# Kernel optimization log

Hardware: AMD Instinct MI355X
Metric: run time of the kernel (lower is better)

The kernel has to match this reference:

```python
import jax, jax.numpy as jnp
import numpy as np

B, D, H, K = 8192, 1280, 16384, 64


def setup_inputs() -> dict:
    key = jax.random.key(0)
    k1, k2, k3 = jax.random.split(key, 3)
    x = jax.random.normal(k1, (B, D), dtype=jnp.float32)
    # encoder weight [hidden_dim, input_dim] (torch Linear layout)
    W_enc = jax.random.normal(k2, (H, D), dtype=jnp.float32) * (1.0 / np.sqrt(D))
    b_enc = jnp.zeros((H,), dtype=jnp.float32)
    # decoder weight [input_dim, hidden_dim], unit-norm columns scaled by 0.1
    W_dec = jax.random.normal(k3, (D, H), dtype=jnp.float32)
    W_dec = 0.1 * W_dec / jnp.linalg.norm(W_dec, axis=0, keepdims=True)
    b_dec = jnp.zeros((D,), dtype=jnp.float32)
    b_pre = jnp.zeros((D,), dtype=jnp.float32)
    return {"x": x, "W_enc": W_enc, "b_enc": b_enc, "W_dec": W_dec,
            "b_dec": b_dec, "b_pre": b_pre, "k": K}


def reference(x, W_enc, b_enc, W_dec, b_dec, b_pre, k):
    # --- encode ---
    x_centered = x - b_pre                                   # [B, D]
    pre = jnp.einsum('bd,hd->bh', x_centered, W_enc) + b_enc  # [B, H]
    vals, idx = jax.lax.top_k(pre, k)                        # [B, k]
    rows = jnp.arange(pre.shape[0])[:, None]                 # [B, 1]
    hidden = jnp.zeros_like(pre).at[rows, idx].set(jax.nn.relu(vals))  # [B, H]
    # --- decode ---
    reconstructed = jnp.einsum('bh,dh->bd', hidden, W_dec) + b_dec + b_pre
    # --- losses ---
    reconstruction_loss = jnp.mean((reconstructed - x) ** 2)
    l0 = jnp.mean(jnp.sum((hidden > 0).astype(jnp.float32), axis=-1))
    sparsity_loss = jnp.array(0.0, dtype=jnp.float32)
    loss = reconstruction_loss
    return reconstructed, hidden, loss, reconstruction_loss, sparsity_loss, l0
```

## Files before the change

### kernel.cpp

```cpp
#include <hip/hip_runtime.h>
#include <hip/hip_bf16.h>

constexpr int K_MAX    = 128;
constexpr int S_MAX    = 128;
constexpr int A_MAX    = 256;
constexpr int CAND_MAX = 512;
constexpr int BM = 128, BN = 128, BKF = 16;
constexpr int NBITER = 42;
constexpr int D_MAX   = 2048;
constexpr int H_FIX   = 16384;

typedef __attribute__((ext_vector_type(8))) short bf16x8;
typedef __attribute__((ext_vector_type(8))) unsigned short u16x8;
typedef __attribute__((ext_vector_type(4))) float f32x4;

__device__ inline unsigned short f2bf(float f) {
  unsigned u = __float_as_uint(f);
  return (unsigned short)((u + 0x7fff + ((u >> 16) & 1)) >> 16);
}
__device__ inline unsigned short key_of(float f) {
  unsigned short b = f2bf(f);
  return b ^ ((b & 0x8000) ? 0xFFFF : 0x8000);
}
__device__ inline float val_of_key(unsigned short kk) {
  unsigned short b = (kk & 0x8000) ? (unsigned short)(kk ^ 0x8000)
                                   : (unsigned short)(kk ^ 0xFFFF);
  return __uint_as_float(((unsigned)b) << 16);
}
__device__ inline float bf2f(unsigned short b) {
  return __uint_as_float(((unsigned)b) << 16);
}

__device__ inline int lds_slot(int r, int c) {
  return ((r >> 1) << 4) | ((r & 1) << 3) | (c ^ ((r >> 1) & 7));
}

__global__ __launch_bounds__(256) void prep_xb(
    const float* __restrict__ x, const float* __restrict__ b_pre,
    unsigned short* __restrict__ Xb, int D, size_t total4)
{
  for (size_t i = blockIdx.x * 256 + threadIdx.x; i < total4; i += (size_t)gridDim.x * 256) {
    const size_t e = i * 4;
    const int d = (int)(e % D);
    float4 xv = *reinterpret_cast<const float4*>(x + e);
    float4 bp = *reinterpret_cast<const float4*>(b_pre + d);
    ushort4 o;
    o.x = f2bf(xv.x - bp.x); o.y = f2bf(xv.y - bp.y);
    o.z = f2bf(xv.z - bp.z); o.w = f2bf(xv.w - bp.w);
    *reinterpret_cast<ushort4*>(Xb + e) = o;
  }
}

__global__ __launch_bounds__(256) void prep_wb(
    const float* __restrict__ W, unsigned short* __restrict__ Wb, size_t total4)
{
  for (size_t i = blockIdx.x * 256 + threadIdx.x; i < total4; i += (size_t)gridDim.x * 256) {
    const size_t e = i * 4;
    float4 wv = *reinterpret_cast<const float4*>(W + e);
    ushort4 o;
    o.x = f2bf(wv.x); o.y = f2bf(wv.y); o.z = f2bf(wv.z); o.w = f2bf(wv.w);
    *reinterpret_cast<ushort4*>(Wb + e) = o;
  }
}

__global__ __launch_bounds__(512, 2) void enc_gemm_bf16(
    const unsigned short* __restrict__ Xb, const unsigned short* __restrict__ Wb,
    const float* __restrict__ b_enc, float* __restrict__ pre, int D, int H)
{
  __shared__ unsigned short As[2][2048 * 8];
  __shared__ unsigned short Bs[2][2048 * 8];
  const int tid  = threadIdx.x;
  const int wave = tid >> 6, lane = tid & 63;
  const int m0 = blockIdx.y * 256, n0 = blockIdx.x * 256;
  const int wm = (wave >> 1) * 64;
  const int wn = (wave & 1) * 128;
  const int l16 = lane & 15, lhi = lane >> 4;

  f32x4 acc[4][8];
#pragma unroll
  for (int i = 0; i < 4; ++i)
#pragma unroll
    for (int j = 0; j < 8; ++j) acc[i][j] = (f32x4){0.f, 0.f, 0.f, 0.f};

  const int NT = D / 64;

  auto stageA = [&](int buf, int h, int kb) {
#pragma unroll
    for (int i = 0; i < 2; ++i) {
      const int idx = i * 512 + wave * 64 + lane;
      const int sr = idx >> 4, u = idx & 15;
      const int r  = (sr << 1) | (u >> 3);
      const int ch = (u & 7) ^ (sr & 7);
      __builtin_amdgcn_global_load_lds(
          (const __attribute__((address_space(1))) unsigned int*)
              (Xb + (size_t)(m0 + h * 128 + r) * D + kb + ch * 8),
          (__attribute__((address_space(3))) unsigned int*)
              (&As[buf][(size_t)(h * 1024 + idx) * 8]), 16, 0, 0);
    }
  };
  auto stageBq = [&](int buf, int q, int kb) {
    const int s  = (q & 1) * 512 + wave * 64 + lane;
    const int sr = s >> 4, u = s & 15;
    const int r  = (sr << 1) | (u >> 3);
    const int ch = (u & 7) ^ (sr & 7);
    __builtin_amdgcn_global_load_lds(
        (const __attribute__((address_space(1))) unsigned int*)
            (Wb + (size_t)(n0 + (q >> 1) * 128 + r) * D + kb + ch * 8),
        (__attribute__((address_space(3))) unsigned int*)
            (&Bs[buf][(size_t)((q >> 1) * 1024 + s) * 8]), 16, 0, 0);
  };
  auto readA = [&](int buf, int mi, int kk) -> bf16x8 {
    const int gr = wm + mi * 16 + l16;
    return *reinterpret_cast<const bf16x8*>(
        &As[buf][(size_t)((gr >> 7) * 1024 + lds_slot(gr & 127, kk * 4 + lhi)) * 8]);
  };
  auto readB = [&](int buf, int ni, int kk) -> bf16x8 {
    const int gr = wn + ni * 16 + l16;
    return *reinterpret_cast<const bf16x8*>(
        &Bs[buf][(size_t)((gr >> 7) * 1024 + lds_slot(gr & 127, kk * 4 + lhi)) * 8]);
  };

  stageA(0, 0, 0); stageA(0, 1, 0);
  stageBq(0, 0, 0); stageBq(0, 2, 0);
  stageBq(0, 1, 0); stageBq(0, 3, 0);

  int cur = 0;
  for (int t = 0; t < NT; ++t) {
    const int nxt = cur ^ 1;
    const int kb1 = (t + 1) * 64;
    const bool more = (t + 1 < NT);

    bf16x8 af[4][2], bf[2][2];

    asm volatile("s_waitcnt vmcnt(2)" ::: "memory");
    __builtin_amdgcn_s_barrier();
#pragma unroll
    for (int mi = 0; mi < 4; ++mi)
#pragma unroll
      for (int kk = 0; kk < 2; ++kk) af[mi][kk] = readA(cur, mi, kk);
#pragma unroll
    for (int j = 0; j < 2; ++j)
#pragma unroll
      for (int kk = 0; kk < 2; ++kk) bf[j][kk] = readB(cur, j, kk);
    if (more) stageA(nxt, 0, kb1);
    __builtin_amdgcn_s_setprio(1);
#pragma unroll
    for (int mi = 0; mi < 4; ++mi)
#pragma unroll
      for (int j = 0; j < 2; ++j)
#pragma unroll
        for (int kk = 0; kk < 2; ++kk)
          acc[mi][j] = __builtin_amdgcn_mfma_f32_16x16x32_bf16(af[mi][kk], bf[j][kk], acc[mi][j], 0, 0, 0);
    __builtin_amdgcn_s_setprio(0);

#pragma unroll
    for (int j = 0; j < 2; ++j)
#pragma unroll
      for (int kk = 0; kk < 2; ++kk) bf[j][kk] = readB(cur, 2 + j, kk);
    if (more) stageA(nxt, 1, kb1);
    __builtin_amdgcn_s_setprio(1);
#pragma unroll
    for (int mi = 0; mi < 4; ++mi)
#pragma unroll
      for (int j = 0; j < 2; ++j)
#pragma unroll
        for (int kk = 0; kk < 2; ++kk)
          acc[mi][2 + j] = __builtin_amdgcn_mfma_f32_16x16x32_bf16(af[mi][kk], bf[j][kk], acc[mi][2 + j], 0, 0, 0);
    __builtin_amdgcn_s_setprio(0);

    if (more) { asm volatile("s_waitcnt vmcnt(4)" ::: "memory"); }
    else      { asm volatile("s_waitcnt vmcnt(0)" ::: "memory"); }
    __builtin_amdgcn_s_barrier();
#pragma unroll
    for (int j = 0; j < 2; ++j)
#pragma unroll
      for (int kk = 0; kk < 2; ++kk) bf[j][kk] = readB(cur, 4 + j, kk);
    if (more) { stageBq(nxt, 0, kb1); stageBq(nxt, 2, kb1); }
    __builtin_amdgcn_s_setprio(1);
#pragma unroll
    for (int mi = 0; mi < 4; ++mi)
#pragma unroll
      for (int j = 0; j < 2; ++j)
#pragma unroll
        for (int kk = 0; kk < 2; ++kk)
          acc[mi][4 + j] = __builtin_amdgcn_mfma_f32_16x16x32_bf16(af[mi][kk], bf[j][kk], acc[mi][4 + j], 0, 0, 0);
    __builtin_amdgcn_s_setprio(0);

#pragma unroll
    for (int j = 0; j < 2; ++j)
#pragma unroll
      for (int kk = 0; kk < 2; ++kk) bf[j][kk] = readB(cur, 6 + j, kk);
    if (more) { stageBq(nxt, 1, kb1); stageBq(nxt, 3, kb1); }
    __builtin_amdgcn_s_setprio(1);
#pragma unroll
    for (int mi = 0; mi < 4; ++mi)
#pragma unroll
      for (int j = 0; j < 2; ++j)
#pragma unroll
        for (int kk = 0; kk < 2; ++kk)
          acc[mi][6 + j] = __builtin_amdgcn_mfma_f32_16x16x32_bf16(af[mi][kk], bf[j][kk], acc[mi][6 + j], 0, 0, 0);
    __builtin_amdgcn_s_setprio(0);

    cur = nxt;
  }

#pragma unroll
  for (int ni = 0; ni < 8; ++ni) {
    const int n = n0 + wn + ni * 16 + l16;
    const float be = b_enc[n];
#pragma unroll
    for (int mi = 0; mi < 4; ++mi) {
      const int mbase = m0 + wm + mi * 16 + lhi * 4;
#pragma unroll
      for (int r = 0; r < 4; ++r) {
        unsigned short* prow = (unsigned short*)(pre + (size_t)(mbase + r) * H);
        prow[n] = key_of(acc[mi][ni][r] + be);
      }
    }
  }
}

__global__ __launch_bounds__(256) void topk_classify_keys(
    float* __restrict__ hidden,
    int* __restrict__ sure_ix, float* __restrict__ sure_val, int* __restrict__ sure_cnt,
    int* __restrict__ amb_ix, int* __restrict__ amb_cnt,
    const int* __restrict__ kptr, float delta)
{
  constexpr int H = H_FIX, NC = H_FIX / (256 * 8);
  __shared__ int hist[4096];
  __shared__ int chunk[256];
  __shared__ int misc[8];

  const int tid = threadIdx.x, b = blockIdx.x;
  const int k = min(*kptr, K_MAX);
  float* hrow = hidden + (size_t)b * H;
  const unsigned short* krow = (const unsigned short*)hrow;

  if (tid < 8) misc[tid] = 0;
  for (int i = tid; i < 4096; i += 256) hist[i] = 0;

  u16x8 kv[NC];
#pragma unroll
  for (int i = 0; i < NC; ++i)
    kv[i] = *reinterpret_cast<const u16x8*>(krow + ((size_t)i * 256 + tid) * 8);
  __syncthreads();

  const float4 z4 = {0.f, 0.f, 0.f, 0.f};
  for (int i = tid; i < (H >> 2); i += 256)
    reinterpret_cast<float4*>(hrow)[i] = z4;

#pragma unroll
  for (int i = 0; i < NC; ++i)
#pragma unroll
    for (int j = 0; j < 8; ++j)
      atomicAdd(&hist[((unsigned)(unsigned short)kv[i][j]) >> 4], 1);
  __syncthreads();

  int csum = 0;
#pragma unroll
  for (int j = 0; j < 16; ++j) csum += hist[tid * 16 + j];
  chunk[tid] = csum;
  __syncthreads();
  int gt = 0;
  for (int j = tid + 1; j < 256; ++j) gt += chunk[j];
  {
    int run = gt;
#pragma unroll
    for (int j = 15; j >= 0; --j) {
      const int hc = hist[tid * 16 + j];
      if (run < k && k <= run + hc) { misc[0] = tid * 16 + j; misc[1] = run; }
      run += hc;
    }
  }
  __syncthreads();
  const int b1 = misc[0];
  if (tid < 16) chunk[tid] = 0;
  __syncthreads();
#pragma unroll
  for (int i = 0; i < NC; ++i)
#pragma unroll
    for (int j = 0; j < 8; ++j) {
      const unsigned kk = (unsigned)(unsigned short)kv[i][j];
      if ((int)(kk >> 4) == b1) atomicAdd(&chunk[kk & 15], 1);
    }
  __syncthreads();
  if (tid == 0) {
    int run = misc[1];
    int K16 = b1 << 4;
    for (int j = 15; j >= 0; --j) {
      const int c = chunk[j];
      if (run < k && k <= run + c) K16 = (b1 << 4) | j;
      run += c;
    }
    const float v_lo = val_of_key((unsigned short)K16);
    const float v_hi = val_of_key((unsigned short)min(K16 + 1, 65535));
    const float ulp = v_hi - v_lo;
    const float vs = v_hi + delta;
    const float va = v_lo - ulp - delta;
    int ks = key_of(vs); if (val_of_key((unsigned short)ks) > vs) --ks;
    int ka = key_of(va); if (val_of_key((unsigned short)ka) < va) ++ka;
    misc[2] = ks; misc[3] = ka;
  }
  __syncthreads();
  const unsigned ks = (unsigned)misc[2], ka = (unsigned)misc[3];

#pragma unroll
  for (int i = 0; i < NC; ++i)
#pragma unroll
    for (int j = 0; j < 8; ++j) {
      const unsigned kk = (unsigned)(unsigned short)kv[i][j];
      if (kk > ks) {
        const int p = atomicAdd(&misc[4], 1);
        if (p < S_MAX) {
          const int h = (i * 256 + tid) * 8 + j;
          sure_ix[(size_t)b * S_MAX + p] = h;
          sure_val[(size_t)b * S_MAX + p] = val_of_key((unsigned short)kk);
        }
      } else if (kk >= ka) {
        const int p = atomicAdd(&misc[5], 1);
        if (p < A_MAX) amb_ix[(size_t)b * A_MAX + p] = (i * 256 + tid) * 8 + j;
      }
    }
  __syncthreads();
  if (tid == 0) {
    sure_cnt[b] = min(misc[4], S_MAX);
    amb_cnt[b]  = min(misc[5], A_MAX);
  }
}

__global__ __launch_bounds__(256) void refine_scatter(
    const float* __restrict__ X, const float* __restrict__ b_pre,
    const float* __restrict__ W, const float* __restrict__ b_enc,
    const int* __restrict__ sure_ix, const float* __restrict__ sure_val,
    const int* __restrict__ sure_cnt,
    const int* __restrict__ amb_ix, const int* __restrict__ amb_cnt,
    const int* __restrict__ kptr,
    float* __restrict__ hidden, int* __restrict__ tk_idx, float* __restrict__ tk_val, int D)
{
  constexpr int H = H_FIX;
  __shared__ float  xr[D_MAX];
  __shared__ double asv[A_MAX];
  __shared__ int    aix[A_MAX];
  const int tid = threadIdx.x, b = blockIdx.x;
  const int k = min(*kptr, K_MAX);
  const int S = min(min(sure_cnt[b], S_MAX), k);
  const int A = min(amb_cnt[b], A_MAX);
  float* hrow = hidden + (size_t)b * H;

  for (int d = tid; d < D; d += 256) xr[d] = X[(size_t)b * D + d] - b_pre[d];
  for (int c = tid; c < A; c += 256) aix[c] = amb_ix[(size_t)b * A_MAX + c];

  for (int i = tid; i < S; i += 256) {
    const int h = sure_ix[(size_t)b * S_MAX + i];
    const float v = sure_val[(size_t)b * S_MAX + i];
    const float rv = (v > 0.f) ? v : 0.f;
    hrow[h] = rv;
    tk_idx[(size_t)b * K_MAX + i] = h;
    tk_val[(size_t)b * K_MAX + i] = rv;
  }
  __syncthreads();

  const int wid = tid >> 6, lane = tid & 63;
  for (int c = wid; c < A; c += 4) {
    const int h = aix[c];
    const float* wr = W + (size_t)h * D;
    double s0 = 0.0, s1 = 0.0;
    int i = lane;
    for (; i + 64 < D; i += 128) {
      s0 += (double)xr[i] * (double)wr[i];
      s1 += (double)xr[i + 64] * (double)wr[i + 64];
    }
    if (i < D) s0 += (double)xr[i] * (double)wr[i];
    double s = s0 + s1;
    for (int off = 32; off; off >>= 1) s += __shfl_xor(s, off);
    if (lane == 0) asv[c] = s + (double)b_enc[h];
  }
  __syncthreads();

  const int m = k - S;
  for (int c = tid; c < A; c += 256) {
    const double v = asv[c];
    const int h = aix[c];
    int r = 0;
    for (int j = 0; j < A; ++j) {
      const double vj = asv[j];
      r += ((vj > v) || (vj == v && aix[j] < h)) ? 1 : 0;
    }
    if (r < m) {
      const float rv = (v > 0.0) ? (float)v : 0.f;
      hrow[h] = rv;
      tk_idx[(size_t)b * K_MAX + S + r] = h;
      tk_val[(size_t)b * K_MAX + S + r] = rv;
    }
  }
}

__global__ __launch_bounds__(256) void enc_gemm_f32(
    const float* __restrict__ X, const float* __restrict__ W,
    const float* __restrict__ b_enc, const float* __restrict__ b_pre,
    float* __restrict__ pre, int D, int H)
{
  __shared__ float As[BKF][BM + 4];
  __shared__ float Bs[BKF][BN + 4];
  const int tid = threadIdx.x;
  const int m0 = blockIdx.y * BM;
  const int n0 = blockIdx.x * BN;
  const int tx = tid & 15, ty = tid >> 4;
  float acc[8][8];
#pragma unroll
  for (int i = 0; i < 8; ++i)
#pragma unroll
    for (int j = 0; j < 8; ++j) acc[i][j] = 0.f;

  for (int kb = 0; kb < D; kb += BKF) {
#pragma unroll
    for (int t = 0; t < 2; ++t) {
      const int f4i = tid + t * 256;
      const int row = f4i >> 2;
      const int kq  = (f4i & 3) << 2;
      float4 xv = *reinterpret_cast<const float4*>(X + (size_t)(m0 + row) * D + kb + kq);
      float4 bp = *reinterpret_cast<const float4*>(b_pre + kb + kq);
      As[kq + 0][row] = xv.x - bp.x; As[kq + 1][row] = xv.y - bp.y;
      As[kq + 2][row] = xv.z - bp.z; As[kq + 3][row] = xv.w - bp.w;
      float4 wv = *reinterpret_cast<const float4*>(W + (size_t)(n0 + row) * D + kb + kq);
      Bs[kq + 0][row] = wv.x; Bs[kq + 1][row] = wv.y;
      Bs[kq + 2][row] = wv.z; Bs[kq + 3][row] = wv.w;
    }
    __syncthreads();
#pragma unroll
    for (int kk = 0; kk < BKF; ++kk) {
      float4 a0 = *reinterpret_cast<const float4*>(&As[kk][ty * 8]);
      float4 a1 = *reinterpret_cast<const float4*>(&As[kk][ty * 8 + 4]);
      float4 b0 = *reinterpret_cast<const float4*>(&Bs[kk][tx * 8]);
      float4 b1 = *reinterpret_cast<const float4*>(&Bs[kk][tx * 8 + 4]);
      float av[8] = {a0.x, a0.y, a0.z, a0.w, a1.x, a1.y, a1.z, a1.w};
      float bv[8] = {b0.x, b0.y, b0.z, b0.w, b1.x, b1.y, b1.z, b1.w};
#pragma unroll
      for (int i = 0; i < 8; ++i)
#pragma unroll
        for (int j = 0; j < 8; ++j) acc[i][j] += av[i] * bv[j];
    }
    __syncthreads();
  }
#pragma unroll
  for (int i = 0; i < 8; ++i) {
    const size_t m = (size_t)(m0 + ty * 8 + i);
#pragma unroll
    for (int j = 0; j < 8; j += 4) {
      const int n = n0 + tx * 8 + j;
      float4 o;
      o.x = acc[i][j + 0] + b_enc[n + 0];
      o.y = acc[i][j + 1] + b_enc[n + 1];
      o.z = acc[i][j + 2] + b_enc[n + 2];
      o.w = acc[i][j + 3] + b_enc[n + 3];
      *reinterpret_cast<float4*>(pre + m * H + n) = o;
    }
  }
}

__global__ __launch_bounds__(256) void topk_refine(
    const float* __restrict__ X, const float* __restrict__ b_pre,
    const float* __restrict__ W, const float* __restrict__ b_enc,
    float* __restrict__ hidden, int* __restrict__ tk_idx, float* __restrict__ tk_val,
    const int* __restrict__ kptr, int D, int H, float margin)
{
  extern __shared__ char smem_raw[];
  double* cand_val = reinterpret_cast<double*>(smem_raw);
  float*  xr       = reinterpret_cast<float*>(cand_val + CAND_MAX);
  int*    cand_idx = reinterpret_cast<int*>(xr + D);
  int*    misc     = cand_idx + CAND_MAX;

  const int tid = threadIdx.x;
  const int b = blockIdx.x;
  const int k = min(*kptr, K_MAX);
  float* hrow = hidden + (size_t)b * H;

  for (int i = tid; i < NBITER + 2; i += 256) misc[i] = 0;
  for (int d = tid; d < D; d += 256) xr[d] = X[(size_t)b * D + d] - b_pre[d];

  float f[64];
#pragma unroll
  for (int i = 0; i < 16; ++i) {
    const int base = i * 1024 + tid * 4;
    float4 v = {-3e38f, -3e38f, -3e38f, -3e38f};
    if (base + 3 < H) v = *reinterpret_cast<const float4*>(hrow + base);
    f[4 * i + 0] = v.x; f[4 * i + 1] = v.y; f[4 * i + 2] = v.z; f[4 * i + 3] = v.w;
  }
  __syncthreads();

  float lo = -1e4f, hi = 1e4f;
  for (int it = 0; it < NBITER; ++it) {
    const float mid = 0.5f * (lo + hi);
    int cnt = 0;
#pragma unroll
    for (int j = 0; j < 64; ++j) cnt += (f[j] >= mid) ? 1 : 0;
    for (int off = 32; off; off >>= 1) cnt += __shfl_xor(cnt, off);
    if ((tid & 63) == 0) atomicAdd(&misc[it], cnt);
    __syncthreads();
    if (misc[it] >= k) lo = mid; else hi = mid;
  }

  const float thresh = lo - margin;
#pragma unroll
  for (int j = 0; j < 64; ++j) {
    if (f[j] >= thresh) {
      const int h = (j >> 2) * 1024 + tid * 4 + (j & 3);
      if (h < H) {
        int pos = atomicAdd(&misc[NBITER], 1);
        if (pos < CAND_MAX) cand_idx[pos] = h;
      }
    }
  }
  __syncthreads();
  const int C = min(misc[NBITER], CAND_MAX);

  const int wid = tid >> 6, lane = tid & 63;
  for (int c = wid; c < C; c += 4) {
    const int h = cand_idx[c];
    const float* wr = W + (size_t)h * D;
    double s = 0.0;
    for (int i = lane; i < D; i += 64) s += (double)xr[i] * (double)wr[i];
    for (int off = 32; off; off >>= 1) s += __shfl_xor(s, off);
    if (lane == 0) cand_val[c] = s + (double)b_enc[h];
  }
  __syncthreads();

  const float4 z4 = {0.f, 0.f, 0.f, 0.f};
  for (int i = tid; i < (H >> 2); i += 256)
    reinterpret_cast<float4*>(hrow)[i] = z4;
  __syncthreads();

  for (int c = tid; c < C; c += 256) {
    const double v = cand_val[c];
    const int h = cand_idx[c];
    int r = 0;
    for (int j = 0; j < C; ++j) {
      const double vj = cand_val[j];
      r += ((vj > v) || (vj == v && cand_idx[j] < h)) ? 1 : 0;
    }
    if (r < k) {
      const float rv = (v > 0.0) ? (float)v : 0.f;
      hrow[h] = rv;
      tk_idx[(size_t)b * K_MAX + r] = h;
      tk_val[(size_t)b * K_MAX + r] = rv;
    }
  }
}

__global__ __launch_bounds__(256) void transpose_wdec_bf16(
    const float* __restrict__ Wsrc, unsigned short* __restrict__ WT, int D, int H)
{
  __shared__ float tile[32][33];
  const int c  = threadIdx.x & 31;
  const int r0 = threadIdx.x >> 5;
  const int h0 = blockIdx.x * 32;
  const int d0 = blockIdx.y * 32;
#pragma unroll
  for (int r = r0; r < 32; r += 8) {
    const int d = d0 + r, h = h0 + c;
    if (d < D && h < H) tile[r][c] = Wsrc[(size_t)d * H + h];
  }
  __syncthreads();
#pragma unroll
  for (int r = r0; r < 32; r += 8) {
    const int h = h0 + r, d = d0 + c;
    if (h < H && d < D) WT[(size_t)h * D + d] = f2bf(tile[c][r]);
  }
}

__global__ __launch_bounds__(256) void decode_loss2(
    const float* __restrict__ X, const float* __restrict__ b_pre,
    const float* __restrict__ b_dec, const unsigned short* __restrict__ WTb,
    const int* __restrict__ tk_idx, const float* __restrict__ tk_val,
    const int* __restrict__ kptr,
    float* __restrict__ recon, double* __restrict__ row_ssq, int D)
{
  __shared__ int   sidx[2][K_MAX];
  __shared__ float sval[2][K_MAX];
  __shared__ double sd[4];
  const int tid = threadIdx.x;
  const int half = tid >> 7, lt = tid & 127;
  const int b = blockIdx.x * 2 + half;
  const int k = min(*kptr, K_MAX);
  if (lt < k) {
    sidx[half][lt] = tk_idx[(size_t)b * K_MAX + lt];
    sval[half][lt] = tk_val[(size_t)b * K_MAX + lt];
  }
  __syncthreads();

  double ssq = 0.0;
  const int D8 = D >> 3;
  for (int dc = lt; dc < D8; dc += 128) {
    const int d = dc * 8;
    float a[8];
#pragma unroll
    for (int q = 0; q < 2; ++q) {
      float4 bd = *reinterpret_cast<const float4*>(b_dec + d + q * 4);
      float4 bp = *reinterpret_cast<const float4*>(b_pre + d + q * 4);
      a[q * 4 + 0] = bd.x + bp.x; a[q * 4 + 1] = bd.y + bp.y;
      a[q * 4 + 2] = bd.z + bp.z; a[q * 4 + 3] = bd.w + bp.w;
    }
#pragma unroll 4
    for (int j = 0; j < k; ++j) {
      const u16x8 w = *reinterpret_cast<const u16x8*>(WTb + (size_t)sidx[half][j] * D + d);
      const float s = sval[half][j];
#pragma unroll
      for (int e = 0; e < 8; ++e) a[e] += s * bf2f((unsigned short)w[e]);
    }
#pragma unroll
    for (int q = 0; q < 2; ++q) {
      float4 o = {a[q * 4 + 0], a[q * 4 + 1], a[q * 4 + 2], a[q * 4 + 3]};
      *reinterpret_cast<float4*>(recon + (size_t)b * D + d + q * 4) = o;
    }
#pragma unroll
    for (int e = 0; e < 8; ++e) {
      const double df = (double)a[e] - (double)X[(size_t)b * D + d + e];
      ssq += df * df;
    }
  }
  for (int off = 32; off; off >>= 1) ssq += __shfl_xor(ssq, off);
  if ((tid & 63) == 0) sd[tid >> 6] = ssq;
  __syncthreads();
  if (tid == 0) row_ssq[blockIdx.x * 2 + 0] = sd[0] + sd[1];
  if (tid == 128) row_ssq[blockIdx.x * 2 + 1] = sd[2] + sd[3];
}

__global__ __launch_bounds__(256) void decode_loss(
    const float* __restrict__ X, const float* __restrict__ b_pre,
    const float* __restrict__ b_dec, const float* __restrict__ Wfull,
    const int* __restrict__ tk_idx, const float* __restrict__ tk_val,
    const int* __restrict__ kptr,
    float* __restrict__ recon, double* __restrict__ row_ssq, int D, int H)
{
  __shared__ int   sidx[K_MAX];
  __shared__ float sval[K_MAX];
  __shared__ double sd[4];
  const int tid = threadIdx.x, b = blockIdx.x;
  const int k = min(*kptr, K_MAX);
  if (tid < k) {
    sidx[tid] = tk_idx[(size_t)b * K_MAX + tid];
    sval[tid] = tk_val[(size_t)b * K_MAX + tid];
  }
  __syncthreads();
  double ssq = 0.0;
  for (int d = tid; d < D; d += 256) {
    float a = b_dec[d] + b_pre[d];
#pragma unroll 4
    for (int j = 0; j < k; ++j) a += sval[j] * Wfull[(size_t)d * H + sidx[j]];
    recon[(size_t)b * D + d] = a;
    const double diff = (double)a - (double)X[(size_t)b * D + d];
    ssq += diff * diff;
  }
  for (int off = 32; off; off >>= 1) ssq += __shfl_xor(ssq, off);
  if ((tid & 63) == 0) sd[tid >> 6] = ssq;
  __syncthreads();
  if (tid == 0) row_ssq[b] = sd[0] + sd[1] + sd[2] + sd[3];
}

__global__ __launch_bounds__(256) void finalize_part(
    const double* __restrict__ row_ssq, const float* __restrict__ tk_val,
    const int* __restrict__ kptr, double* __restrict__ part_s, int* __restrict__ part_c,
    int Bdim, int rows_per_blk)
{
  __shared__ double sd[4];
  __shared__ int si[4];
  const int tid = threadIdx.x;
  const int k = min(*kptr, K_MAX);
  const int b0 = blockIdx.x * rows_per_blk;
  const int b1 = min(b0 + rows_per_blk, Bdim);
  double s = 0.0;
  for (int i = b0 + tid; i < b1; i += 256) s += row_ssq[i];
  int cnt = 0;
  const int total = (b1 - b0) * k;
  for (int i = tid; i < total; i += 256) {
    const int bb = b0 + i / k, j = i - (i / k) * k;
    cnt += (tk_val[(size_t)bb * K_MAX + j] > 0.f) ? 1 : 0;
  }
  for (int off = 32; off; off >>= 1) { s += __shfl_xor(s, off); cnt += __shfl_xor(cnt, off); }
  if ((tid & 63) == 0) { sd[tid >> 6] = s; si[tid >> 6] = cnt; }
  __syncthreads();
  if (tid == 0) {
    part_s[blockIdx.x] = sd[0] + sd[1] + sd[2] + sd[3];
    part_c[blockIdx.x] = si[0] + si[1] + si[2] + si[3];
  }
}

__global__ __launch_bounds__(64) void finalize_k2(
    const double* __restrict__ part_s, const int* __restrict__ part_c,
    float* __restrict__ scalars, int nparts, int Bdim, int D)
{
  const int tid = threadIdx.x;
  double s = (tid < nparts) ? part_s[tid] : 0.0;
  int cnt = (tid < nparts) ? part_c[tid] : 0;
  for (int off = 32; off; off >>= 1) { s += __shfl_xor(s, off); cnt += __shfl_xor(cnt, off); }
  if (tid == 0) {
    const double rl = s / ((double)Bdim * (double)D);
    scalars[0] = (float)rl;
    scalars[1] = (float)rl;
    scalars[2] = 0.f;
    scalars[3] = (float)((double)cnt / Bdim);
  }
}

extern "C" void kernel_launch(void* const* d_in, const int* in_sizes, int n_in,
                              void* d_out, int out_size, void* d_ws, size_t ws_size,
                              hipStream_t stream)
{
  const float* x     = (const float*)d_in[0];
  const float* W_enc = (const float*)d_in[1];
  const float* b_enc = (const float*)d_in[2];
  const float* W_dec = (const float*)d_in[3];
  const float* b_dec = (const float*)d_in[4];
  const float* b_pre = (const float*)d_in[5];
  const int*   kptr  = (const int*)d_in[6];

  const int D = in_sizes[4];
  const int H = in_sizes[2];
  const int B = in_sizes[0] / D;

  float* recon   = (float*)d_out;
  float* hidden  = recon + (size_t)B * D;
  float* scalars = hidden + (size_t)B * H;

  size_t off = 0;
  int* tk_idx = (int*)((char*)d_ws + off);        off += (size_t)B * K_MAX * sizeof(int);
  float* tk_val = (float*)((char*)d_ws + off);    off += (size_t)B * K_MAX * sizeof(float);
  off = (off + 7) & ~(size_t)7;
  double* row_ssq = (double*)((char*)d_ws + off); off += (size_t)B * sizeof(double);
  double* part_s = (double*)((char*)d_ws + off);  off += 64 * sizeof(double);
  int* part_c = (int*)((char*)d_ws + off);        off += 64 * sizeof(int);
  off = (off + 7) & ~(size_t)7;

  unsigned short* Xb = (unsigned short*)((char*)d_ws + off);
  off += (size_t)B * D * sizeof(unsigned short);
  unsigned short* Wb = (unsigned short*)((char*)d_ws + off);
  off += (size_t)H * D * sizeof(unsigned short);
  unsigned short* WTb = (unsigned short*)((char*)d_ws + off);
  off += (size_t)D * H * sizeof(unsigned short);

  int* sure_ix = (int*)((char*)d_ws + off);       off += (size_t)B * S_MAX * sizeof(int);
  float* sure_val = (float*)((char*)d_ws + off);  off += (size_t)B * S_MAX * sizeof(float);
  int* sure_cnt = (int*)((char*)d_ws + off);      off += (size_t)B * sizeof(int);
  int* amb_ix = (int*)((char*)d_ws + off);        off += (size_t)B * A_MAX * sizeof(int);
  int* amb_cnt = (int*)((char*)d_ws + off);       off += (size_t)B * sizeof(int);
  const int useFAST = (off <= ws_size) ? 1 : 0;

  const bool fast_ok = (D % 64 == 0) && (D <= D_MAX) &&
                       (H == H_FIX) && (B % 256 == 0);

  if (useFAST && fast_ok) {
    const size_t tx4 = (size_t)B * D / 4, tw4 = (size_t)H * D / 4;
    prep_xb<<<2048, 256, 0, stream>>>(x, b_pre, Xb, D, tx4);
    prep_wb<<<2048, 256, 0, stream>>>(W_enc, Wb, tw4);
    dim3 gg(H / 256, B / 256);
    enc_gemm_bf16<<<gg, 512, 0, stream>>>(Xb, Wb, b_enc, hidden, D, H);
    topk_classify_keys<<<B, 256, 0, stream>>>(hidden, sure_ix, sure_val, sure_cnt,
                                              amb_ix, amb_cnt, kptr, 0.05f);
    refine_scatter<<<B, 256, 0, stream>>>(x, b_pre, W_enc, b_enc,
                                          sure_ix, sure_val, sure_cnt,
                                          amb_ix, amb_cnt, kptr,
                                          hidden, tk_idx, tk_val, D);
    transpose_wdec_bf16<<<dim3((H + 31) / 32, (D + 31) / 32), 256, 0, stream>>>(W_dec, WTb, D, H);
    decode_loss2<<<B / 2, 256, 0, stream>>>(x, b_pre, b_dec, WTb,
                                            tk_idx, tk_val, kptr, recon, row_ssq, D);
  } else {
    dim3 gg(H / BN, B / BM);
    enc_gemm_f32<<<gg, 256, 0, stream>>>(x, W_enc, b_enc, b_pre, hidden, D, H);
    const size_t sh = CAND_MAX * sizeof(double) + (size_t)D * sizeof(float)
                    + CAND_MAX * sizeof(int) + (NBITER + 8) * sizeof(int);
    topk_refine<<<B, 256, sh, stream>>>(x, b_pre, W_enc, b_enc, hidden,
                                        tk_idx, tk_val, kptr, D, H, 1e-3f);
    decode_loss<<<B, 256, 0, stream>>>(x, b_pre, b_dec, W_dec,
                                       tk_idx, tk_val, kptr, recon, row_ssq, D, H);
  }

  const int rpb = (B + 63) / 64;
  finalize_part<<<64, 256, 0, stream>>>(row_ssq, tk_val, kptr, part_s, part_c, B, rpb);
  finalize_k2<<<1, 64, 0, stream>>>(part_s, part_c, scalars, 64, B, D);
}
```

Before: 998.8 us.

## Load encoder GEMM A operand directly to registers, stage only B in LDS

The encoder GEMM no longer stages the X tile in shared memory. Each wave now loads its A fragments straight from global memory into registers, double-buffered across two register sets with the main loop unrolled by two. Only W stays in LDS, which halves LDS use and may let two blocks share a CU, and the per-tile sync collapses to one __syncthreads. In exchange, waves sharing the same rows fetch duplicate, less-coalesced global loads, register pressure rises, and the fast-path guard now requires D to be a multiple of 128.

```diff
diff --git a/kernel.cpp b/kernel.cpp
--- a/kernel.cpp
+++ b/kernel.cpp
@@ -67,7 +67,6 @@
     const unsigned short* __restrict__ Xb, const unsigned short* __restrict__ Wb,
     const float* __restrict__ b_enc, float* __restrict__ pre, int D, int H)
 {
-  __shared__ unsigned short As[2][2048 * 8];
   __shared__ unsigned short Bs[2][2048 * 8];
   const int tid  = threadIdx.x;
   const int wave = tid >> 6, lane = tid & 63;
@@ -84,35 +83,27 @@
 
   const int NT = D / 64;
 
-  auto stageA = [&](int buf, int h, int kb) {
-#pragma unroll
-    for (int i = 0; i < 2; ++i) {
-      const int idx = i * 512 + wave * 64 + lane;
-      const int sr = idx >> 4, u = idx & 15;
+  auto loadA = [&](bf16x8 (&dst)[4][2], int kb) {
+#pragma unroll
+    for (int mi = 0; mi < 4; ++mi)
+#pragma unroll
+      for (int kk = 0; kk < 2; ++kk)
+        dst[mi][kk] = *reinterpret_cast<const bf16x8*>(
+            Xb + (size_t)(m0 + wm + mi * 16 + l16) * D + kb + kk * 32 + lhi * 8);
+  };
+  auto stageB = [&](int buf, int kb) {
+#pragma unroll
+    for (int q = 0; q < 4; ++q) {
+      const int s  = (q & 1) * 512 + wave * 64 + lane;
+      const int sr = s >> 4, u = s & 15;
       const int r  = (sr << 1) | (u >> 3);
       const int ch = (u & 7) ^ (sr & 7);
       __builtin_amdgcn_global_load_lds(
           (const __attribute__((address_space(1))) unsigned int*)
-              (Xb + (size_t)(m0 + h * 128 + r) * D + kb + ch * 8),
+              (Wb + (size_t)(n0 + (q >> 1) * 128 + r) * D + kb + ch * 8),
           (__attribute__((address_space(3))) unsigned int*)
-              (&As[buf][(size_t)(h * 1024 + idx) * 8]), 16, 0, 0);
-    }
-  };
-  auto stageBq = [&](int buf, int q, int kb) {
-    const int s  = (q & 1) * 512 + wave * 64 + lane;
-    const int sr = s >> 4, u = s & 15;
-    const int r  = (sr << 1) | (u >> 3);
-    const int ch = (u & 7) ^ (sr & 7);
-    __builtin_amdgcn_global_load_lds(
-        (const __attribute__((address_space(1))) unsigned int*)
-            (Wb + (size_t)(n0 + (q >> 1) * 128 + r) * D + kb + ch * 8),
-        (__attribute__((address_space(3))) unsigned int*)
-            (&Bs[buf][(size_t)((q >> 1) * 1024 + s) * 8]), 16, 0, 0);
-  };
-  auto readA = [&](int buf, int mi, int kk) -> bf16x8 {
-    const int gr = wm + mi * 16 + l16;
-    return *reinterpret_cast<const bf16x8*>(
-        &As[buf][(size_t)((gr >> 7) * 1024 + lds_slot(gr & 127, kk * 4 + lhi)) * 8]);
+              (&Bs[buf][(size_t)((q >> 1) * 1024 + s) * 8]), 16, 0, 0);
+    }
   };
   auto readB = [&](int buf, int ni, int kk) -> bf16x8 {
     const int gr = wn + ni * 16 + l16;
@@ -120,29 +111,35 @@
         &Bs[buf][(size_t)((gr >> 7) * 1024 + lds_slot(gr & 127, kk * 4 + lhi)) * 8]);
   };
 
-  stageA(0, 0, 0); stageA(0, 1, 0);
-  stageBq(0, 0, 0); stageBq(0, 2, 0);
-  stageBq(0, 1, 0); stageBq(0, 3, 0);
-
-  int cur = 0;
-  for (int t = 0; t < NT; ++t) {
-    const int nxt = cur ^ 1;
-    const int kb1 = (t + 1) * 64;
+  bf16x8 afA[4][2], afB[4][2];
+  loadA(afA, 0);
+  stageB(0, 0);
+
+  auto tile = [&](bf16x8 (&ac)[4][2], bf16x8 (&an)[4][2], int t) {
     const bool more = (t + 1 < NT);
-
-    bf16x8 af[4][2], bf[2][2];
-
-    asm volatile("s_waitcnt vmcnt(2)" ::: "memory");
-    __builtin_amdgcn_s_barrier();
+    const int buf = t & 1;
+    __syncthreads();
+    bf16x8 bfr[2][2];
+
+#pragma unroll
+    for (int j = 0; j < 2; ++j)
+#pragma unroll
+      for (int kk = 0; kk < 2; ++kk) bfr[j][kk] = readB(buf, j, kk);
+    __builtin_amdgcn_s_setprio(1);
 #pragma unroll
     for (int mi = 0; mi < 4; ++mi)
 #pragma unroll
-      for (int kk = 0; kk < 2; ++kk) af[mi][kk] = readA(cur, mi, kk);
+      for (int j = 0; j < 2; ++j)
+#pragma unroll
+        for (int kk = 0; kk < 2; ++kk)
+          acc[mi][j] = __builtin_amdgcn_mfma_f32_16x16x32_bf16(ac[mi][kk], bfr[j][kk], acc[mi][j], 0, 0, 0);
+    __builtin_amdgcn_s_setprio(0);
+    if (more) loadA(an, (t + 1) * 64);
+
 #pragma unroll
     for (int j = 0; j < 2; ++j)
 #pragma unroll
-      for (int kk = 0; kk < 2; ++kk) bf[j][kk] = readB(cur, j, kk);
-    if (more) stageA(nxt, 0, kb1);
+      for (int kk = 0; kk < 2; ++kk) bfr[j][kk] = readB(buf, 2 + j, kk);
     __builtin_amdgcn_s_setprio(1);
 #pragma unroll
     for (int mi = 0; mi < 4; ++mi)
@@ -150,14 +147,14 @@
       for (int j = 0; j < 2; ++j)
 #pragma unroll
         for (int kk = 0; kk < 2; ++kk)
-          acc[mi][j] = __builtin_amdgcn_mfma_f32_16x16x32_bf16(af[mi][kk], bf[j][kk], acc[mi][j], 0, 0, 0);
+          acc[mi][2 + j] = __builtin_amdgcn_mfma_f32_16x16x32_bf16(ac[mi][kk], bfr[j][kk], acc[mi][2 + j], 0, 0, 0);
     __builtin_amdgcn_s_setprio(0);
+    if (more) stageB((t + 1) & 1, (t + 1) * 64);
 
 #pragma unroll
     for (int j = 0; j < 2; ++j)
 #pragma unroll
-      for (int kk = 0; kk < 2; ++kk) bf[j][kk] = readB(cur, 2 + j, kk);
-    if (more) stageA(nxt, 1, kb1);
+      for (int kk = 0; kk < 2; ++kk) bfr[j][kk] = readB(buf, 4 + j, kk);
     __builtin_amdgcn_s_setprio(1);
 #pragma unroll
     for (int mi = 0; mi < 4; ++mi)
@@ -165,17 +162,13 @@
       for (int j = 0; j < 2; ++j)
 #pragma unroll
         for (int kk = 0; kk < 2; ++kk)
-          acc[mi][2 + j] = __builtin_amdgcn_mfma_f32_16x16x32_bf16(af[mi][kk], bf[j][kk], acc[mi][2 + j], 0, 0, 0);
+          acc[mi][4 + j] = __builtin_amdgcn_mfma_f32_16x16x32_bf16(ac[mi][kk], bfr[j][kk], acc[mi][4 + j], 0, 0, 0);
     __builtin_amdgcn_s_setprio(0);
 
-    if (more) { asm volatile("s_waitcnt vmcnt(4)" ::: "memory"); }
-    else      { asm volatile("s_waitcnt vmcnt(0)" ::: "memory"); }
-    __builtin_amdgcn_s_barrier();
 #pragma unroll
     for (int j = 0; j < 2; ++j)
 #pragma unroll
-      for (int kk = 0; kk < 2; ++kk) bf[j][kk] = readB(cur, 4 + j, kk);
-    if (more) { stageBq(nxt, 0, kb1); stageBq(nxt, 2, kb1); }
+      for (int kk = 0; kk < 2; ++kk) bfr[j][kk] = readB(buf, 6 + j, kk);
     __builtin_amdgcn_s_setprio(1);
 #pragma unroll
     for (int mi = 0; mi < 4; ++mi)
@@ -183,25 +176,13 @@
       for (int j = 0; j < 2; ++j)
 #pragma unroll
         for (int kk = 0; kk < 2; ++kk)
-          acc[mi][4 + j] = __builtin_amdgcn_mfma_f32_16x16x32_bf16(af[mi][kk], bf[j][kk], acc[mi][4 + j], 0, 0, 0);
+          acc[mi][6 + j] = __builtin_amdgcn_mfma_f32_16x16x32_bf16(ac[mi][kk], bfr[j][kk], acc[mi][6 + j], 0, 0, 0);
     __builtin_amdgcn_s_setprio(0);
-
-#pragma unroll
-    for (int j = 0; j < 2; ++j)
-#pragma unroll
-      for (int kk = 0; kk < 2; ++kk) bf[j][kk] = readB(cur, 6 + j, kk);
-    if (more) { stageBq(nxt, 1, kb1); stageBq(nxt, 3, kb1); }
-    __builtin_amdgcn_s_setprio(1);
-#pragma unroll
-    for (int mi = 0; mi < 4; ++mi)
-#pragma unroll
-      for (int j = 0; j < 2; ++j)
-#pragma unroll
-        for (int kk = 0; kk < 2; ++kk)
-          acc[mi][6 + j] = __builtin_amdgcn_mfma_f32_16x16x32_bf16(af[mi][kk], bf[j][kk], acc[mi][6 + j], 0, 0, 0);
-    __builtin_amdgcn_s_setprio(0);
-
-    cur = nxt;
+  };
+
+  for (int t = 0; t < NT; t += 2) {
+    tile(afA, afB, t);
+    if (t + 1 < NT) tile(afB, afA, t + 1);
   }
 
 #pragma unroll
@@ -745,7 +726,7 @@
   int* amb_cnt = (int*)((char*)d_ws + off);       off += (size_t)B * sizeof(int);
   const int useFAST = (off <= ws_size) ? 1 : 0;
 
-  const bool fast_ok = (D % 64 == 0) && (D <= D_MAX) &&
+  const bool fast_ok = (D % 128 == 0) && (D <= D_MAX) &&
                        (H == H_FIX) && (B % 256 == 0);
 
   if (useFAST && fast_ok) {
```

Result: slower. 1.175 ms (+17.7%).
